# Performance work log

Hardware: AMD Instinct MI355X
Metric: run time of the kernel (lower is better)

The kernel has to match this reference:

```python
import jax, jax.numpy as jnp
import numpy as np

E = 3_200_000  # edges
N = 100_000    # atoms
B = 64         # graphs


def setup_inputs() -> dict:
    key = jax.random.key(0)
    k1, k2, k3, k4 = jax.random.split(key, 4)
    disp = jax.random.normal(k1, (E, 3), dtype=jnp.float32)
    edge_w = jax.random.uniform(k2, (E,), dtype=jnp.float32)
    edge_index = jax.random.randint(k3, (2, E), 0, N)
    batch = jnp.sort(jax.random.randint(k4, (N,), 0, B))
    return {"disp": disp, "edge_w": edge_w, "edge_index": edge_index,
            "batch": batch, "num_graphs": B}


def reference(disp, edge_w, edge_index, batch, num_graphs):
    n_atoms = batch.shape[0]

    # Surrogate differentiable energy of disp (stands in for the upstream model):
    # E = sum_e w_e * ||disp_e||^2. pairwise_force = -dE/ddisp via autodiff,
    # matching torch.autograd.grad(energy, disp).
    def energy_fn(d):
        return jnp.sum(edge_w * jnp.sum(d * d, axis=-1))

    pairwise_force = -jax.grad(energy_fn)(disp)  # (E, 3)

    # Per-edge virial outer product: (E, 3, 3)
    virial_e = disp[:, :, None] * pairwise_force[:, None, :]

    # Double scatter-add to atoms (both endpoints), then scatter to graphs.
    v_atom = (jax.ops.segment_sum(virial_e, edge_index[0], num_segments=n_atoms)
              + jax.ops.segment_sum(virial_e, edge_index[1], num_segments=n_atoms))  # (N,3,3)
    v_graph = jax.ops.segment_sum(v_atom, batch, num_segments=num_graphs)  # (B,3,3)
    return v_graph
```

## Files before the change

### kernel.cpp

```cpp
#include <hip/hip_runtime.h>
#include <hip/hip_fp8.h>


#define NG 64
#define NCOMP 6
#define NPART (NG * NCOMP)
#define RED1_BLOCKS 64
#define MFMA_BLOCKS 1024
#define WPB 4
#define MROWB 80
#define DROWB 80
#define DTROWS 6

typedef unsigned char  u8_t;
typedef unsigned int   u32_t;
typedef __attribute__((ext_vector_type(2))) long long long2_t;
typedef __attribute__((ext_vector_type(4))) float f32x4;

__device__ __forceinline__ int eperm(int e) {
    return (((e >> 3) & 3) << 4) | (((e >> 5) & 1) << 3) | (e & 7);
}

__device__ __forceinline__ u8_t f2fp8(float f) {
    return (u8_t)__hip_cvt_float_to_fp8(f, __HIP_SATFINITE, __HIP_E4M3);
}

__device__ __forceinline__ void lds_add(float* p, float v) {
    __hip_atomic_fetch_add(p, v, __ATOMIC_RELAXED, __HIP_MEMORY_SCOPE_WORKGROUP);
}

__device__ __forceinline__ int gsearch(const int* Bs, int a, float rcpN) {
    int g = (int)((float)a * rcpN);
    g = g > 63 ? 63 : g;
    while (Bs[g] > a) --g;
    while (Bs[g + 1] <= a) ++g;
    return g;
}

__global__ __launch_bounds__(256) void virial_mfma(
    const float* __restrict__ disp, const float* __restrict__ edge_w,
    const int* __restrict__ edge_index, const int* __restrict__ batch,
    float* __restrict__ partials, int E, int N, float rcpN)
{
    __shared__ u8_t Msh[WPB][NG * MROWB];
    __shared__ u8_t Dsh[WPB][DTROWS * DROWB];
    __shared__ int  Bs[65];

    const int lane = threadIdx.x & 63;
    const int wave = threadIdx.x >> 6;
    u8_t* Mw = Msh[wave];
    u8_t* Dw = Dsh[wave];

    if (threadIdx.x < 65) {
        int g = threadIdx.x;
        int lo = 0, len = N;
        while (len > 0) {
            int half = len >> 1;
            int mid  = lo + half;
            if (batch[mid] < g) { lo = mid + 1; len -= half + 1; }
            else                { len = half; }
        }
        Bs[g] = lo;
    }
    {
        u32_t* p = (u32_t*)Mw;
        for (int i = lane; i < NG * MROWB / 4; i += 64) p[i] = 0u;
        u32_t* q = (u32_t*)Dw;
        for (int i = lane; i < DTROWS * DROWB / 4; i += 64) q[i] = 0u;
    }
    __syncthreads();

    f32x4 acc0 = {0,0,0,0}, acc1 = {0,0,0,0}, acc2 = {0,0,0,0}, acc3 = {0,0,0,0};
    const int ngroups = (E + 63) >> 6;
    const int gstride = (int)gridDim.x * WPB;
    const int c_l  = lane & 15;
    const int k4   = lane >> 4;
    const int mcol = eperm(lane);
    const int drow = (c_l < DTROWS) ? c_l : (DTROWS - 1);
    int pg0 = 0, pg1 = 0;

#define LOADG(G, W, X, Y, Z, S, T) do {                                     \
        int e_  = (G) * 64 + lane;                                          \
        int ec_ = e_ < E ? e_ : E - 1;                                      \
        W = (e_ < E) ? edge_w[ec_] : 0.f;       \
        X = disp[ec_ * 3 + 0];                                              \
        Y = disp[ec_ * 3 + 1];                                              \
        Z = disp[ec_ * 3 + 2];                                              \
        S = edge_index[ec_];                                                \
        T = edge_index[E + ec_];                                            \
    } while (0)

#define COMPUTEG(W, X, Y, Z, S, T) do {                                     \
        const int g0_ = gsearch(Bs, S, rcpN);                               \
        const int g1_ = gsearch(Bs, T, rcpN);                               \
        Mw[pg0 * MROWB + mcol] = 0;                                         \
        Mw[pg1 * MROWB + mcol] = 0;                                         \
        Mw[g0_ * MROWB + mcol] = 0x38u;                                     \
        Mw[g1_ * MROWB + mcol] = (g1_ == g0_) ? 0x40u : 0x38u;              \
        pg0 = g0_; pg1 = g1_;                                               \
        float cw_ = -2.f * W;                                               \
        Dw[0 * DROWB + mcol] = f2fp8(cw_ * X * X);                          \
        Dw[1 * DROWB + mcol] = f2fp8(cw_ * X * Y);                          \
        Dw[2 * DROWB + mcol] = f2fp8(cw_ * X * Z);                          \
        Dw[3 * DROWB + mcol] = f2fp8(cw_ * Y * Y);                          \
        Dw[4 * DROWB + mcol] = f2fp8(cw_ * Y * Z);                          \
        Dw[5 * DROWB + mcol] = f2fp8(cw_ * Z * Z);                          \
        long2_t bf_ = *(const long2_t*)&Dw[drow * DROWB + k4 * 16];         \
        long2_t a0_ = *(const long2_t*)&Mw[( 0 + c_l) * MROWB + k4 * 16];   \
        long2_t a1_ = *(const long2_t*)&Mw[(16 + c_l) * MROWB + k4 * 16];   \
        long2_t a2_ = *(const long2_t*)&Mw[(32 + c_l) * MROWB + k4 * 16];   \
        long2_t a3_ = *(const long2_t*)&Mw[(48 + c_l) * MROWB + k4 * 16];   \
        acc0 = __builtin_amdgcn_mfma_f32_16x16x32_fp8_fp8(a0_[0], bf_[0], acc0, 0, 0, 0); \
        acc1 = __builtin_amdgcn_mfma_f32_16x16x32_fp8_fp8(a1_[0], bf_[0], acc1, 0, 0, 0); \
        acc2 = __builtin_amdgcn_mfma_f32_16x16x32_fp8_fp8(a2_[0], bf_[0], acc2, 0, 0, 0); \
        acc3 = __builtin_amdgcn_mfma_f32_16x16x32_fp8_fp8(a3_[0], bf_[0], acc3, 0, 0, 0); \
        acc0 = __builtin_amdgcn_mfma_f32_16x16x32_fp8_fp8(a0_[1], bf_[1], acc0, 0, 0, 0); \
        acc1 = __builtin_amdgcn_mfma_f32_16x16x32_fp8_fp8(a1_[1], bf_[1], acc1, 0, 0, 0); \
        acc2 = __builtin_amdgcn_mfma_f32_16x16x32_fp8_fp8(a2_[1], bf_[1], acc2, 0, 0, 0); \
        acc3 = __builtin_amdgcn_mfma_f32_16x16x32_fp8_fp8(a3_[1], bf_[1], acc3, 0, 0, 0); \
    } while (0)

    int grp = (int)blockIdx.x * WPB + wave;

    float wA = 0.f, xA = 0.f, yA = 0.f, zA = 0.f;
    int   sA = 0, tA = 0;
    float wB = 0.f, xB = 0.f, yB = 0.f, zB = 0.f;
    int   sB = 0, tB = 0;
    if (grp < ngroups)           LOADG(grp,           wA, xA, yA, zA, sA, tA);
    if (grp + gstride < ngroups) LOADG(grp + gstride, wB, xB, yB, zB, sB, tB);

    while (grp < ngroups) {
        COMPUTEG(wA, xA, yA, zA, sA, tA);
        if (grp + 2 * gstride < ngroups)
            LOADG(grp + 2 * gstride, wA, xA, yA, zA, sA, tA);
        grp += gstride;
        if (grp >= ngroups) break;

        COMPUTEG(wB, xB, yB, zB, sB, tB);
        if (grp + 2 * gstride < ngroups)
            LOADG(grp + 2 * gstride, wB, xB, yB, zB, sB, tB);
        grp += gstride;
    }
#undef LOADG
#undef COMPUTEG

    __syncthreads();
    float* Ow = (float*)Mw;
    if (c_l < NCOMP) {
#pragma unroll
        for (int r = 0; r < 4; ++r) {
            Ow[( 0 + k4 * 4 + r) * NCOMP + c_l] = acc0[r];
            Ow[(16 + k4 * 4 + r) * NCOMP + c_l] = acc1[r];
            Ow[(32 + k4 * 4 + r) * NCOMP + c_l] = acc2[r];
            Ow[(48 + k4 * 4 + r) * NCOMP + c_l] = acc3[r];
        }
    }
    __syncthreads();
    for (int i = threadIdx.x; i < NPART; i += blockDim.x) {
        float s = ((const float*)Msh[0])[i] + ((const float*)Msh[1])[i]
                + ((const float*)Msh[2])[i] + ((const float*)Msh[3])[i];
        partials[(size_t)blockIdx.x * NPART + i] = s;
    }
}

__global__ __launch_bounds__(NPART) void reduce1_kernel(
    const float* __restrict__ partials, float* __restrict__ partials2, int nblk)
{
    int i = threadIdx.x, j = blockIdx.x;
    float s = 0.f;
    for (int b = j; b < nblk; b += RED1_BLOCKS)
        s += partials[(size_t)b * NPART + i];
    partials2[(size_t)j * NPART + i] = s;
}

__global__ __launch_bounds__(NPART) void reduce2_kernel(
    const float* __restrict__ partials2, float* __restrict__ dst)
{
    int i = threadIdx.x;
    float s = 0.f;
#pragma unroll
    for (int j = 0; j < RED1_BLOCKS; ++j)
        s += partials2[(size_t)j * NPART + i];
    int g = i / NCOMP, c = i % NCOMP;
    int r   = (c < 3) ? 0 : ((c < 5) ? 1 : 2);
    int col = (c < 3) ? c : ((c < 5) ? c - 2 : 2);
    dst[g * 9 + r * 3 + col] = s;
    if (r != col) dst[g * 9 + col * 3 + r] = s;
}

__global__ void zero_out_kernel(float* __restrict__ out, int n) {
    int i = blockIdx.x * blockDim.x + threadIdx.x;
    if (i < n) out[i] = 0.f;
}

__global__ __launch_bounds__(256) void virial_atomic(
    const float* __restrict__ disp, const float* __restrict__ edge_w,
    const int* __restrict__ edge_index, const int* __restrict__ batch,
    float* __restrict__ out, int E)
{
    __shared__ float acc[NG * 7];
    for (int i = threadIdx.x; i < NG * 7; i += blockDim.x) acc[i] = 0.f;
    __syncthreads();
    int tid = blockIdx.x * blockDim.x + threadIdx.x;
    int stride = gridDim.x * blockDim.x;
    for (int e = tid; e < E; e += stride) {
        float d0 = disp[e*3], d1 = disp[e*3+1], d2 = disp[e*3+2];
        float c = -2.f * edge_w[e];
        int g0 = batch[edge_index[e]], g1 = batch[edge_index[E + e]];
        float v[6] = {c*d0*d0, c*d0*d1, c*d0*d2, c*d1*d1, c*d1*d2, c*d2*d2};
#pragma unroll
        for (int k = 0; k < 6; ++k) {
            lds_add(&acc[g0*7+k], v[k]);
            lds_add(&acc[g1*7+k], v[k]);
        }
    }
    __syncthreads();
    for (int i = threadIdx.x; i < NG * 9; i += blockDim.x) {
        int g = i / 9, ij = i % 9, r = ij / 3, cc = ij % 3;
        int lo = r < cc ? r : cc, hi = r < cc ? cc : r;
        int comp = (lo == 0) ? hi : ((lo == 1) ? 2 + hi : 5);
        __hip_atomic_fetch_add(&out[i], acc[g*7+comp], __ATOMIC_RELAXED, __HIP_MEMORY_SCOPE_AGENT);
    }
}

extern "C" void kernel_launch(void* const* d_in, const int* in_sizes, int n_in,
                              void* d_out, int out_size, void* d_ws, size_t ws_size,
                              hipStream_t stream) {
    const float* disp       = (const float*)d_in[0];
    const float* edge_w     = (const float*)d_in[1];
    const int*   edge_index = (const int*)d_in[2];
    const int*   batch      = (const int*)d_in[3];
    float*       out        = (float*)d_out;
    const int E = in_sizes[1];
    const int N = in_sizes[3];
    const float rcpN = (float)NG / (float)N;

    const size_t need = (size_t)(MFMA_BLOCKS + RED1_BLOCKS) * NPART * sizeof(float);

    if (ws_size >= need) {
        float* pm = (float*)d_ws;
        float* p2 = pm + (size_t)MFMA_BLOCKS * NPART;

        virial_mfma<<<MFMA_BLOCKS, 256, 0, stream>>>(disp, edge_w, edge_index,
                                                     batch, pm, E, N, rcpN);
        reduce1_kernel<<<RED1_BLOCKS, NPART, 0, stream>>>(pm, p2, MFMA_BLOCKS);
        reduce2_kernel<<<1, NPART, 0, stream>>>(p2, out);
    } else {
        zero_out_kernel<<<1, 256, 0, stream>>>(out, NG * 9);
        virial_atomic<<<2048, 256, 0, stream>>>(disp, edge_w, edge_index, batch, out, E);
    }
}
```

Measured before the change: 37.14 us.

## Double-buffer LDS tiles to overlap one-hot/fp8 writes with MFMA of previous group

Each wave's graph one-hot matrix and fp8 virial tile now use two LDS buffers. The writes for group N go to one buffer while the MFMAs consume group N-1 from the other, so the LDS write-then-read dependency within one iteration is broken. The grid also shrinks from 1024 to 768 blocks to offset the doubled LDS footprint, which may lower occupancy. This adds extra MFMA bookkeeping at the loop tail.

```diff
diff --git a/kernel.cpp b/kernel.cpp
--- a/kernel.cpp
+++ b/kernel.cpp
@@ -6,7 +6,7 @@
 #define NCOMP 6
 #define NPART (NG * NCOMP)
 #define RED1_BLOCKS 64
-#define MFMA_BLOCKS 1024
+#define MFMA_BLOCKS 768
 #define WPB 4
 #define MROWB 80
 #define DROWB 80
@@ -42,14 +42,18 @@
     const int* __restrict__ edge_index, const int* __restrict__ batch,
     float* __restrict__ partials, int E, int N, float rcpN)
 {
-    __shared__ u8_t Msh[WPB][NG * MROWB];
-    __shared__ u8_t Dsh[WPB][DTROWS * DROWB];
+    __shared__ u8_t Msh0[WPB][NG * MROWB];
+    __shared__ u8_t Msh1[WPB][NG * MROWB];
+    __shared__ u8_t Dsh0[WPB][DTROWS * DROWB];
+    __shared__ u8_t Dsh1[WPB][DTROWS * DROWB];
     __shared__ int  Bs[65];
 
     const int lane = threadIdx.x & 63;
     const int wave = threadIdx.x >> 6;
-    u8_t* Mw = Msh[wave];
-    u8_t* Dw = Dsh[wave];
+    u8_t* Mw0 = Msh0[wave];
+    u8_t* Mw1 = Msh1[wave];
+    u8_t* Dw0 = Dsh0[wave];
+    u8_t* Dw1 = Dsh1[wave];
 
     if (threadIdx.x < 65) {
         int g = threadIdx.x;
@@ -63,10 +67,12 @@
         Bs[g] = lo;
     }
     {
-        u32_t* p = (u32_t*)Mw;
-        for (int i = lane; i < NG * MROWB / 4; i += 64) p[i] = 0u;
-        u32_t* q = (u32_t*)Dw;
-        for (int i = lane; i < DTROWS * DROWB / 4; i += 64) q[i] = 0u;
+        u32_t* p0 = (u32_t*)Mw0;
+        u32_t* p1 = (u32_t*)Mw1;
+        for (int i = lane; i < NG * MROWB / 4; i += 64) { p0[i] = 0u; p1[i] = 0u; }
+        u32_t* q0 = (u32_t*)Dw0;
+        u32_t* q1 = (u32_t*)Dw1;
+        for (int i = lane; i < DTROWS * DROWB / 4; i += 64) { q0[i] = 0u; q1[i] = 0u; }
     }
     __syncthreads();
 
@@ -77,7 +83,6 @@
     const int k4   = lane >> 4;
     const int mcol = eperm(lane);
     const int drow = (c_l < DTROWS) ? c_l : (DTROWS - 1);
-    int pg0 = 0, pg1 = 0;
 
 #define LOADG(G, W, X, Y, Z, S, T) do {                                     \
         int e_  = (G) * 64 + lane;                                          \
@@ -90,26 +95,29 @@
         T = edge_index[E + ec_];                                            \
     } while (0)
 
-#define COMPUTEG(W, X, Y, Z, S, T) do {                                     \
+#define WRITEG(MW, DW, PG0, PG1, W, X, Y, Z, S, T) do {                     \
         const int g0_ = gsearch(Bs, S, rcpN);                               \
         const int g1_ = gsearch(Bs, T, rcpN);                               \
-        Mw[pg0 * MROWB + mcol] = 0;                                         \
-        Mw[pg1 * MROWB + mcol] = 0;                                         \
-        Mw[g0_ * MROWB + mcol] = 0x38u;                                     \
-        Mw[g1_ * MROWB + mcol] = (g1_ == g0_) ? 0x40u : 0x38u;              \
-        pg0 = g0_; pg1 = g1_;                                               \
+        MW[PG0 * MROWB + mcol] = 0;                                         \
+        MW[PG1 * MROWB + mcol] = 0;                                         \
+        MW[g0_ * MROWB + mcol] = 0x38u;                                     \
+        MW[g1_ * MROWB + mcol] = (g1_ == g0_) ? 0x40u : 0x38u;              \
+        PG0 = g0_; PG1 = g1_;                                               \
         float cw_ = -2.f * W;                                               \
-        Dw[0 * DROWB + mcol] = f2fp8(cw_ * X * X);                          \
-        Dw[1 * DROWB + mcol] = f2fp8(cw_ * X * Y);                          \
-        Dw[2 * DROWB + mcol] = f2fp8(cw_ * X * Z);                          \
-        Dw[3 * DROWB + mcol] = f2fp8(cw_ * Y * Y);                          \
-        Dw[4 * DROWB + mcol] = f2fp8(cw_ * Y * Z);                          \
-        Dw[5 * DROWB + mcol] = f2fp8(cw_ * Z * Z);                          \
-        long2_t bf_ = *(const long2_t*)&Dw[drow * DROWB + k4 * 16];         \
-        long2_t a0_ = *(const long2_t*)&Mw[( 0 + c_l) * MROWB + k4 * 16];   \
-        long2_t a1_ = *(const long2_t*)&Mw[(16 + c_l) * MROWB + k4 * 16];   \
-        long2_t a2_ = *(const long2_t*)&Mw[(32 + c_l) * MROWB + k4 * 16];   \
-        long2_t a3_ = *(const long2_t*)&Mw[(48 + c_l) * MROWB + k4 * 16];   \
+        DW[0 * DROWB + mcol] = f2fp8(cw_ * X * X);                          \
+        DW[1 * DROWB + mcol] = f2fp8(cw_ * X * Y);                          \
+        DW[2 * DROWB + mcol] = f2fp8(cw_ * X * Z);                          \
+        DW[3 * DROWB + mcol] = f2fp8(cw_ * Y * Y);                          \
+        DW[4 * DROWB + mcol] = f2fp8(cw_ * Y * Z);                          \
+        DW[5 * DROWB + mcol] = f2fp8(cw_ * Z * Z);                          \
+    } while (0)
+
+#define MFMAG(MW, DW) do {                                                  \
+        long2_t bf_ = *(const long2_t*)&DW[drow * DROWB + k4 * 16];         \
+        long2_t a0_ = *(const long2_t*)&MW[( 0 + c_l) * MROWB + k4 * 16];   \
+        long2_t a1_ = *(const long2_t*)&MW[(16 + c_l) * MROWB + k4 * 16];   \
+        long2_t a2_ = *(const long2_t*)&MW[(32 + c_l) * MROWB + k4 * 16];   \
+        long2_t a3_ = *(const long2_t*)&MW[(48 + c_l) * MROWB + k4 * 16];   \
         acc0 = __builtin_amdgcn_mfma_f32_16x16x32_fp8_fp8(a0_[0], bf_[0], acc0, 0, 0, 0); \
         acc1 = __builtin_amdgcn_mfma_f32_16x16x32_fp8_fp8(a1_[0], bf_[0], acc1, 0, 0, 0); \
         acc2 = __builtin_amdgcn_mfma_f32_16x16x32_fp8_fp8(a2_[0], bf_[0], acc2, 0, 0, 0); \
@@ -129,23 +137,37 @@
     if (grp < ngroups)           LOADG(grp,           wA, xA, yA, zA, sA, tA);
     if (grp + gstride < ngroups) LOADG(grp + gstride, wB, xB, yB, zB, sB, tB);
 
+    int pg0a = 0, pg1a = 0, pg0b = 0, pg1b = 0;
+    bool first = true;
+    bool lastA = true;
+
     while (grp < ngroups) {
-        COMPUTEG(wA, xA, yA, zA, sA, tA);
+        WRITEG(Mw0, Dw0, pg0a, pg1a, wA, xA, yA, zA, sA, tA);
         if (grp + 2 * gstride < ngroups)
             LOADG(grp + 2 * gstride, wA, xA, yA, zA, sA, tA);
+        if (!first) MFMAG(Mw1, Dw1);
+        first = false;
+        lastA = true;
         grp += gstride;
         if (grp >= ngroups) break;
 
-        COMPUTEG(wB, xB, yB, zB, sB, tB);
+        WRITEG(Mw1, Dw1, pg0b, pg1b, wB, xB, yB, zB, sB, tB);
         if (grp + 2 * gstride < ngroups)
             LOADG(grp + 2 * gstride, wB, xB, yB, zB, sB, tB);
+        MFMAG(Mw0, Dw0);
+        lastA = false;
         grp += gstride;
     }
+    if (!first) {
+        if (lastA) MFMAG(Mw0, Dw0);
+        else       MFMAG(Mw1, Dw1);
+    }
 #undef LOADG
-#undef COMPUTEG
-
-    __syncthreads();
-    float* Ow = (float*)Mw;
+#undef WRITEG
+#undef MFMAG
+
+    __syncthreads();
+    float* Ow = (float*)Mw0;
     if (c_l < NCOMP) {
 #pragma unroll
         for (int r = 0; r < 4; ++r) {
@@ -157,8 +179,8 @@
     }
     __syncthreads();
     for (int i = threadIdx.x; i < NPART; i += blockDim.x) {
-        float s = ((const float*)Msh[0])[i] + ((const float*)Msh[1])[i]
-                + ((const float*)Msh[2])[i] + ((const float*)Msh[3])[i];
+        float s = ((const float*)Msh0[0])[i] + ((const float*)Msh0[1])[i]
+                + ((const float*)Msh0[2])[i] + ((const float*)Msh0[3])[i];
         partials[(size_t)blockIdx.x * NPART + i] = s;
     }
 }
```

After: 37.90 us. +2.0%, slower.

## Load four consecutive edges per lane with vectorized float4/int4 loads

Applied to the files above, without the earlier changes.

Each wave now processes macro-groups of 256 edges, with every lane loading four consecutive edges through 16-byte vector loads of weights, displacements and indices. The old scheme issued scalar loads per edge, including stride-3 displacement loads. The loop keeps one macro-group prefetched ahead instead of two alternating groups. Assigning a lane's edges contiguously changes which edges share each MFMA sub-group and raises register pressure, which may lower occupancy.

```diff
diff --git a/kernel.cpp b/kernel.cpp
--- a/kernel.cpp
+++ b/kernel.cpp
@@ -71,45 +71,65 @@
     __syncthreads();
 
     f32x4 acc0 = {0,0,0,0}, acc1 = {0,0,0,0}, acc2 = {0,0,0,0}, acc3 = {0,0,0,0};
-    const int ngroups = (E + 63) >> 6;
-    const int gstride = (int)gridDim.x * WPB;
+    const int nmacros = (E + 255) >> 8;
+    const int mstride = (int)gridDim.x * WPB;
     const int c_l  = lane & 15;
     const int k4   = lane >> 4;
     const int mcol = eperm(lane);
     const int drow = (c_l < DTROWS) ? c_l : (DTROWS - 1);
     int pg0 = 0, pg1 = 0;
 
-#define LOADG(G, W, X, Y, Z, S, T) do {                                     \
-        int e_  = (G) * 64 + lane;                                          \
-        int ec_ = e_ < E ? e_ : E - 1;                                      \
-        W = (e_ < E) ? edge_w[ec_] : 0.f;       \
-        X = disp[ec_ * 3 + 0];                                              \
-        Y = disp[ec_ * 3 + 1];                                              \
-        Z = disp[ec_ * 3 + 2];                                              \
-        S = edge_index[ec_];                                                \
-        T = edge_index[E + ec_];                                            \
+#define LOADM(MAC, W4, DA, DB, DC, S4, T4) do {                               \
+        int eb_ = (MAC) * 256 + 4 * lane;                                     \
+        if (((MAC) + 1) * 256 <= E) {                                         \
+            W4 = *(const float4*)&edge_w[eb_];                                \
+            DA = *(const float4*)&disp[eb_ * 3 + 0];                          \
+            DB = *(const float4*)&disp[eb_ * 3 + 4];                          \
+            DC = *(const float4*)&disp[eb_ * 3 + 8];                          \
+            S4 = *(const int4*)&edge_index[eb_];                              \
+            T4 = *(const int4*)&edge_index[E + eb_];                          \
+        } else {                                                              \
+            float w_[4], x_[12]; int s_[4], t_[4];                            \
+            _Pragma("unroll")                                                 \
+            for (int k_ = 0; k_ < 4; ++k_) {                                  \
+                int e_  = eb_ + k_;                                           \
+                int ec_ = e_ < E ? e_ : E - 1;                                \
+                w_[k_] = (e_ < E) ? edge_w[ec_] : 0.f;                        \
+                x_[3*k_+0] = disp[ec_*3+0];                                   \
+                x_[3*k_+1] = disp[ec_*3+1];                                   \
+                x_[3*k_+2] = disp[ec_*3+2];                                   \
+                s_[k_] = edge_index[ec_];                                     \
+                t_[k_] = edge_index[E + ec_];                                 \
+            }                                                                 \
+            W4 = make_float4(w_[0], w_[1], w_[2], w_[3]);                     \
+            DA = make_float4(x_[0], x_[1], x_[2],  x_[3]);                    \
+            DB = make_float4(x_[4], x_[5], x_[6],  x_[7]);                    \
+            DC = make_float4(x_[8], x_[9], x_[10], x_[11]);                   \
+            S4 = make_int4(s_[0], s_[1], s_[2], s_[3]);                       \
+            T4 = make_int4(t_[0], t_[1], t_[2], t_[3]);                       \
+        }                                                                     \
     } while (0)
 
-#define COMPUTEG(W, X, Y, Z, S, T) do {                                     \
-        const int g0_ = gsearch(Bs, S, rcpN);                               \
-        const int g1_ = gsearch(Bs, T, rcpN);                               \
-        Mw[pg0 * MROWB + mcol] = 0;                                         \
-        Mw[pg1 * MROWB + mcol] = 0;                                         \
-        Mw[g0_ * MROWB + mcol] = 0x38u;                                     \
-        Mw[g1_ * MROWB + mcol] = (g1_ == g0_) ? 0x40u : 0x38u;              \
-        pg0 = g0_; pg1 = g1_;                                               \
-        float cw_ = -2.f * W;                                               \
-        Dw[0 * DROWB + mcol] = f2fp8(cw_ * X * X);                          \
-        Dw[1 * DROWB + mcol] = f2fp8(cw_ * X * Y);                          \
-        Dw[2 * DROWB + mcol] = f2fp8(cw_ * X * Z);                          \
-        Dw[3 * DROWB + mcol] = f2fp8(cw_ * Y * Y);                          \
-        Dw[4 * DROWB + mcol] = f2fp8(cw_ * Y * Z);                          \
-        Dw[5 * DROWB + mcol] = f2fp8(cw_ * Z * Z);                          \
-        long2_t bf_ = *(const long2_t*)&Dw[drow * DROWB + k4 * 16];         \
-        long2_t a0_ = *(const long2_t*)&Mw[( 0 + c_l) * MROWB + k4 * 16];   \
-        long2_t a1_ = *(const long2_t*)&Mw[(16 + c_l) * MROWB + k4 * 16];   \
-        long2_t a2_ = *(const long2_t*)&Mw[(32 + c_l) * MROWB + k4 * 16];   \
-        long2_t a3_ = *(const long2_t*)&Mw[(48 + c_l) * MROWB + k4 * 16];   \
+#define SUBG(W, X, Y, Z, S, T) do {                                           \
+        const int g0_ = gsearch(Bs, S, rcpN);                                 \
+        const int g1_ = gsearch(Bs, T, rcpN);                                 \
+        Mw[pg0 * MROWB + mcol] = 0;                                           \
+        Mw[pg1 * MROWB + mcol] = 0;                                           \
+        Mw[g0_ * MROWB + mcol] = 0x38u;                                       \
+        Mw[g1_ * MROWB + mcol] = (g1_ == g0_) ? 0x40u : 0x38u;                \
+        pg0 = g0_; pg1 = g1_;                                                 \
+        float cw_ = -2.f * W;                                                 \
+        Dw[0 * DROWB + mcol] = f2fp8(cw_ * X * X);                            \
+        Dw[1 * DROWB + mcol] = f2fp8(cw_ * X * Y);                            \
+        Dw[2 * DROWB + mcol] = f2fp8(cw_ * X * Z);                            \
+        Dw[3 * DROWB + mcol] = f2fp8(cw_ * Y * Y);                            \
+        Dw[4 * DROWB + mcol] = f2fp8(cw_ * Y * Z);                            \
+        Dw[5 * DROWB + mcol] = f2fp8(cw_ * Z * Z);                            \
+        long2_t bf_ = *(const long2_t*)&Dw[drow * DROWB + k4 * 16];           \
+        long2_t a0_ = *(const long2_t*)&Mw[( 0 + c_l) * MROWB + k4 * 16];     \
+        long2_t a1_ = *(const long2_t*)&Mw[(16 + c_l) * MROWB + k4 * 16];     \
+        long2_t a2_ = *(const long2_t*)&Mw[(32 + c_l) * MROWB + k4 * 16];     \
+        long2_t a3_ = *(const long2_t*)&Mw[(48 + c_l) * MROWB + k4 * 16];     \
         acc0 = __builtin_amdgcn_mfma_f32_16x16x32_fp8_fp8(a0_[0], bf_[0], acc0, 0, 0, 0); \
         acc1 = __builtin_amdgcn_mfma_f32_16x16x32_fp8_fp8(a1_[0], bf_[0], acc1, 0, 0, 0); \
         acc2 = __builtin_amdgcn_mfma_f32_16x16x32_fp8_fp8(a2_[0], bf_[0], acc2, 0, 0, 0); \
@@ -120,29 +140,27 @@
         acc3 = __builtin_amdgcn_mfma_f32_16x16x32_fp8_fp8(a3_[1], bf_[1], acc3, 0, 0, 0); \
     } while (0)
 
-    int grp = (int)blockIdx.x * WPB + wave;
-
-    float wA = 0.f, xA = 0.f, yA = 0.f, zA = 0.f;
-    int   sA = 0, tA = 0;
-    float wB = 0.f, xB = 0.f, yB = 0.f, zB = 0.f;
-    int   sB = 0, tB = 0;
-    if (grp < ngroups)           LOADG(grp,           wA, xA, yA, zA, sA, tA);
-    if (grp + gstride < ngroups) LOADG(grp + gstride, wB, xB, yB, zB, sB, tB);
-
-    while (grp < ngroups) {
-        COMPUTEG(wA, xA, yA, zA, sA, tA);
-        if (grp + 2 * gstride < ngroups)
-            LOADG(grp + 2 * gstride, wA, xA, yA, zA, sA, tA);
-        grp += gstride;
-        if (grp >= ngroups) break;
-
-        COMPUTEG(wB, xB, yB, zB, sB, tB);
-        if (grp + 2 * gstride < ngroups)
-            LOADG(grp + 2 * gstride, wB, xB, yB, zB, sB, tB);
-        grp += gstride;
-    }
-#undef LOADG
-#undef COMPUTEG
+    int mac = (int)blockIdx.x * WPB + wave;
+
+    float4 nw4 = {0,0,0,0}, ndA = {0,0,0,0}, ndB = {0,0,0,0}, ndC = {0,0,0,0};
+    int4   ns4 = {0,0,0,0}, nt4 = {0,0,0,0};
+    if (mac < nmacros) LOADM(mac, nw4, ndA, ndB, ndC, ns4, nt4);
+
+    while (mac < nmacros) {
+        const float4 w4 = nw4, dA = ndA, dB = ndB, dC = ndC;
+        const int4   s4 = ns4, t4 = nt4;
+        const int nxt = mac + mstride;
+        if (nxt < nmacros) LOADM(nxt, nw4, ndA, ndB, ndC, ns4, nt4);
+
+        SUBG(w4.x, dA.x, dA.y, dA.z, s4.x, t4.x);
+        SUBG(w4.y, dA.w, dB.x, dB.y, s4.y, t4.y);
+        SUBG(w4.z, dB.z, dB.w, dC.x, s4.z, t4.z);
+        SUBG(w4.w, dC.y, dC.z, dC.w, s4.w, t4.w);
+
+        mac = nxt;
+    }
+#undef LOADM
+#undef SUBG
 
     __syncthreads();
     float* Ow = (float*)Mw;
```

New measurement: 39.71 us. +6.9%, slower.
